# Kernel optimization log

Measured on AMD Instinct MI355X. Metric: run time of the kernel, lower is better.

## Reference

```python
import jax, jax.numpy as jnp
import numpy as np

N = 50000
E = 1_600_000
IN_C = 128
OUT_C = 128


def _glorot(key, shape):
    fan_in, fan_out = shape[0], shape[1]
    s = jnp.sqrt(6.0 / (fan_in + fan_out))
    return jax.random.uniform(key, shape, jnp.float32, -s, s)


def setup_inputs() -> dict:
    key = jax.random.key(0)
    ks = jax.random.split(key, 32)
    inp = {
        'X': jax.random.normal(ks[0], (N, IN_C), jnp.float32),
        'edge_index': jax.random.randint(ks[1], (2, E), 0, N, jnp.int64),
        'edge_weight': jax.random.uniform(ks[2], (E,), jnp.float32),
        'H': jax.random.normal(ks[3], (N, OUT_C), jnp.float32),
        'C': jax.random.normal(ks[4], (N, OUT_C), jnp.float32),
    }
    i = 5
    for g in ('i', 'f', 'c', 'o'):
        inp[f'Wx_{g}'] = _glorot(ks[i], (IN_C, OUT_C)); i += 1
        inp[f'bx_{g}'] = jnp.zeros((OUT_C,), jnp.float32)
        inp[f'Wh_{g}'] = _glorot(ks[i], (OUT_C, OUT_C)); i += 1
        inp[f'bh_{g}'] = jnp.zeros((OUT_C,), jnp.float32)
    for g in ('i', 'f', 'o'):
        inp[f'w_c_{g}'] = _glorot(ks[i], (1, OUT_C)); i += 1
    for g in ('i', 'f', 'c', 'o'):
        inp[f'b_{g}'] = jnp.zeros((1, OUT_C), jnp.float32)
    return inp


def reference(X, edge_index, edge_weight, H, C,
              Wx_i, bx_i, Wh_i, bh_i,
              Wx_f, bx_f, Wh_f, bh_f,
              Wx_c, bx_c, Wh_c, bh_c,
              Wx_o, bx_o, Wh_o, bh_o,
              w_c_i, w_c_f, w_c_o,
              b_i, b_f, b_c, b_o):
    n = X.shape[0]
    src, dst = edge_index[0], edge_index[1]
    # GCN normalization (add_self_loops=False): deg from destination (in-degree)
    deg = jax.ops.segment_sum(edge_weight, dst, num_segments=n)
    dis = jnp.where(deg > 0, jax.lax.rsqrt(jnp.where(deg > 0, deg, 1.0)), 0.0)
    norm = dis[src] * edge_weight * dis[dst]  # [E]

    def gcn(x, W, b):
        xw = x @ W                       # [n, OUT_C]
        msg = xw[src] * norm[:, None]    # gather + scale, [E, OUT_C]
        return jax.ops.segment_sum(msg, dst, num_segments=n) + b

    I = jax.nn.sigmoid(gcn(X, Wx_i, bx_i) + gcn(H, Wh_i, bh_i) + w_c_i * C + b_i)
    Fg = jax.nn.sigmoid(gcn(X, Wx_f, bx_f) + gcn(H, Wh_f, bh_f) + w_c_f * C + b_f)
    T = jnp.tanh(gcn(X, Wx_c, bx_c) + gcn(H, Wh_c, bh_c) + b_c)
    Cn = Fg * C + I * T
    O = jax.nn.sigmoid(gcn(X, Wx_o, bx_o) + gcn(H, Wh_o, bh_o) + w_c_o * Cn + b_o)
    Hn = O * jnp.tanh(Cn)
    return Hn, Cn
```

## Files before the change

### kernel.cpp

```cpp
#include <hip/hip_runtime.h>

__device__ __forceinline__ float bf2f(unsigned short u){
    union { unsigned int i; float f; } v; v.i = ((unsigned int)u) << 16; return v.f;
}
__device__ __forceinline__ unsigned short f2bf(float f){
    union { unsigned int i; float f; } v; v.f = f;
    unsigned int i = v.i;
    unsigned int r = i + 0x7FFFu + ((i >> 16) & 1u);
    return (unsigned short)(r >> 16);
}
__device__ __forceinline__ float sigm(float x){ return 1.0f / (1.0f + __expf(-x)); }

__device__ __forceinline__ float ldsel(const void* p, size_t idx, int fF){
    float r;
    if (fF) r = ((const float*)p)[idx];
    else    r = bf2f(((const unsigned short*)p)[idx]);
    return r;
}

typedef __attribute__((ext_vector_type(8))) short s8v;
typedef __attribute__((ext_vector_type(4))) float f4v;

__global__ void k_detect(const unsigned short* __restrict__ X,
                         const int* __restrict__ ei, int* __restrict__ flags){
    __shared__ int cnt, nz;
    if (threadIdx.x == 0){ cnt = 0; nz = 0; }
    __syncthreads();
    int ok = 0;
    for (int i = threadIdx.x; i < 2048; i += 256){
        int e = (X[i] >> 7) & 0xFF;
        if (e >= 96 && e <= 160) ok++;
    }
    atomicAdd(&cnt, ok);
    int nzl = 0;
    for (int i = threadIdx.x; i < 128; i += 256)
        if (ei[2*i + 1] != 0) nzl++;
    atomicAdd(&nz, nzl);
    __syncthreads();
    if (threadIdx.x == 0){
        flags[0] = (cnt < 1843) ? 1 : 0;
        flags[1] = (nz == 0)   ? 1 : 0;
    }
}

struct PackArgs {
    const void* Wx[4];
    const void* Wh[4];
    const void* bx[4];
    const void* bh[4];
};

__global__ void k_fused1(const void* __restrict__ X, const void* __restrict__ H,
                         uint4* __restrict__ XHb128,
                         const int* __restrict__ ei, const void* __restrict__ ew,
                         unsigned long long* __restrict__ pk,
                         int* __restrict__ off,
                         PackArgs pa, unsigned short* __restrict__ Bp,
                         float* __restrict__ bias,
                         const int* __restrict__ flags,
                         int nbC, int nbT, int E, int N){
    int b = blockIdx.x;
    int fF = flags[0];
    if (b < nbC){
        int base = b*2048 + threadIdx.x;
        int fI = flags[1];
        int dd[8]; unsigned long long pv[8];
#pragma unroll
        for (int k = 0; k < 8; k++){
            int e = base + k*256;
            dd[k] = -1; pv[k] = 0;
            if (e < E){
                dd[k] = fI ? ei[2*(size_t)E + 2*(size_t)e] : ei[(size_t)E + e];
                float w = ldsel(ew, e, fF);
                unsigned int wfix = (unsigned int)(w * 16777216.0f + 0.5f);
                pv[k] = (1ULL << 32) | (unsigned long long)wfix;
            }
        }
#pragma unroll
        for (int k = 0; k < 8; k++){
            int e = base + k*256;
            if (e < E && (unsigned)dd[k] < (unsigned)N){
                unsigned long long old = atomicAdd(&pk[dd[k]], pv[k]);
                off[e] = (int)(old >> 32);
            }
        }
    } else if (b < nbC + nbT){
        int t = (b - nbC)*256 + threadIdx.x;
        if (t >= N*32) return;
        int n = t >> 5, i = t & 31;
        int q = (i < 16) ? i : i - 16;
        uint4 o;
        if (fF){
            const float4* src = (const float4*)((i < 16) ? X : H);
            float4 a = src[(size_t)n*32 + q*2];
            float4 bb = src[(size_t)n*32 + q*2 + 1];
            o.x = ((unsigned int)f2bf(a.y) << 16) | f2bf(a.x);
            o.y = ((unsigned int)f2bf(a.w) << 16) | f2bf(a.z);
            o.z = ((unsigned int)f2bf(bb.y) << 16) | f2bf(bb.x);
            o.w = ((unsigned int)f2bf(bb.w) << 16) | f2bf(bb.z);
        } else {
            const uint4* src = (const uint4*)((i < 16) ? X : H);
            o = src[(size_t)n*16 + q];
        }
        XHb128[(size_t)n*32 + i] = o;
    } else {
        int t = (b - nbC - nbT)*256 + threadIdx.x;
        if (t < 4*8*8*64*8){
            int j    =  t        & 7;
            int lane = (t >> 3)  & 63;
            int kb   = (t >> 9)  & 7;
            int ct   = (t >> 12) & 7;
            int g    = (t >> 15) & 3;
            int k   = kb*32 + (lane >> 4)*8 + j;
            int col = ct*16 + (lane & 15);
            const void* p; size_t idx;
            if (k < 128){ p = pa.Wx[g]; idx = (size_t)k*128 + col; }
            else        { p = pa.Wh[g]; idx = (size_t)(k-128)*128 + col; }
            unsigned short v;
            if (fF) v = f2bf(((const float*)p)[idx]);
            else    v = ((const unsigned short*)p)[idx];
            Bp[t] = v;
        }
        if (t < 512){
            int g = t >> 7, c = t & 127;
            bias[t] = ldsel(pa.bx[g], c, fF) + ldsel(pa.bh[g], c, fF);
        }
    }
}

__global__ void k_scanA(const unsigned long long* __restrict__ pk,
                        int* __restrict__ bsum, int n){
    __shared__ int sh[256];
    int t = threadIdx.x, i = blockIdx.x * 256 + t;
    sh[t] = (i < n) ? (int)(pk[i] >> 32) : 0;
    __syncthreads();
    for (int o = 128; o > 0; o >>= 1){
        if (t < o) sh[t] += sh[t + o];
        __syncthreads();
    }
    if (t == 0) bsum[blockIdx.x] = sh[0];
}
__global__ void k_scanB(const int* __restrict__ bsum, int* __restrict__ bsumoff, int nb){
    __shared__ int sh[256];
    int t = threadIdx.x;
    int v = (t < nb) ? bsum[t] : 0;
    sh[t] = v;
    __syncthreads();
    for (int o = 1; o < 256; o <<= 1){
        int u = (t >= o) ? sh[t - o] : 0;
        __syncthreads();
        sh[t] += u;
        __syncthreads();
    }
    bsumoff[t] = sh[t] - v;
}
__global__ void k_scanC(const unsigned long long* __restrict__ pk,
                        const int* __restrict__ bsumoff,
                        int* __restrict__ rowstart, float* __restrict__ dis, int n){
    __shared__ int sh[256];
    int t = threadIdx.x, i = blockIdx.x * 256 + t;
    unsigned long long pv = (i < n) ? pk[i] : 0ULL;
    int v = (int)(pv >> 32);
    sh[t] = v;
    __syncthreads();
    for (int o = 1; o < 256; o <<= 1){
        int u = (t >= o) ? sh[t - o] : 0;
        __syncthreads();
        sh[t] += u;
        __syncthreads();
    }
    int incl = sh[t];
    if (i < n){
        rowstart[i] = bsumoff[blockIdx.x] + incl - v;
        float dg = (float)(unsigned int)pv * (1.0f/16777216.0f);
        dis[i] = (dg > 0.f) ? rsqrtf(dg) : 0.f;
    }
    if (i == n-1)  rowstart[n] = bsumoff[blockIdx.x] + incl;
}

__global__ void k_scatter(const int* __restrict__ ei, const void* __restrict__ ew,
                          const int* __restrict__ rowstart, const int* __restrict__ off,
                          int2* __restrict__ recs, const int* __restrict__ flags,
                          int E, int N){
    int base = blockIdx.x*1024 + threadIdx.x;
    int fF = flags[0], fI = flags[1];
    int ss[4], dd[4], oo[4]; float wv[4];
#pragma unroll
    for (int k = 0; k < 4; k++){
        int e = base + k*256;
        dd[k] = -1; ss[k] = 0; wv[k] = 0.f; oo[k] = 0;
        if (e < E){
            if (fI){ ss[k] = ei[2*(size_t)e]; dd[k] = ei[2*(size_t)E + 2*(size_t)e]; }
            else   { ss[k] = ei[e];           dd[k] = ei[(size_t)E + e]; }
            oo[k] = off[e];
            if ((unsigned)ss[k] < (unsigned)N) wv[k] = ldsel(ew, e, fF);
            else ss[k] = 0;
        }
    }
#pragma unroll
    for (int k = 0; k < 4; k++){
        if ((unsigned)dd[k] < (unsigned)N){
            int2 r; r.x = ss[k]; r.y = __float_as_int(wv[k]);
            recs[rowstart[dd[k]] + oo[k]] = r;
        }
    }
}

__global__ __launch_bounds__(256)
void k_gather(const int2* __restrict__ recs, const int* __restrict__ rowstart,
              const float* __restrict__ dis, const uint4* __restrict__ XHb128,
              uint4* __restrict__ AXH128, int N){
    int node = (blockIdx.x * 256 + threadIdx.x) >> 6;
    int lane = threadIdx.x & 63;
    if (node >= N) return;
    int half = lane >> 5;
    int sub  = lane & 31;
    int beg = rowstart[node], end = rowstart[node + 1];
    float disd = dis[node];
    float a0=0.f,a1=0.f,a2=0.f,a3=0.f,a4=0.f,a5=0.f,a6=0.f,a7=0.f;

#define ACC8(v, n)                                              \
    a0 += (n) * bf2f((unsigned short)((v).x & 0xffff));         \
    a1 += (n) * bf2f((unsigned short)((v).x >> 16));            \
    a2 += (n) * bf2f((unsigned short)((v).y & 0xffff));         \
    a3 += (n) * bf2f((unsigned short)((v).y >> 16));            \
    a4 += (n) * bf2f((unsigned short)((v).z & 0xffff));         \
    a5 += (n) * bf2f((unsigned short)((v).z >> 16));            \
    a6 += (n) * bf2f((unsigned short)((v).w & 0xffff));         \
    a7 += (n) * bf2f((unsigned short)((v).w >> 16));

    int i = beg;
    for (; i + 7 < end; i += 8){
        int2 rA = recs[i     + half];
        int2 rB = recs[i + 2 + half];
        int2 rC = recs[i + 4 + half];
        int2 rD = recs[i + 6 + half];
        uint4 vA = XHb128[(size_t)rA.x*32 + sub];
        uint4 vB = XHb128[(size_t)rB.x*32 + sub];
        uint4 vC = XHb128[(size_t)rC.x*32 + sub];
        uint4 vD = XHb128[(size_t)rD.x*32 + sub];
        float nA = dis[rA.x] * __int_as_float(rA.y) * disd;
        float nB = dis[rB.x] * __int_as_float(rB.y) * disd;
        float nC = dis[rC.x] * __int_as_float(rC.y) * disd;
        float nD = dis[rD.x] * __int_as_float(rD.y) * disd;
        ACC8(vA, nA);
        ACC8(vB, nB);
        ACC8(vC, nC);
        ACC8(vD, nD);
    }
    for (; i + 1 < end; i += 2){
        int2 rA = recs[i + half];
        uint4 vA = XHb128[(size_t)rA.x*32 + sub];
        float nA = dis[rA.x] * __int_as_float(rA.y) * disd;
        ACC8(vA, nA);
    }
    if (i < end){
        int2 rA = recs[i];
        uint4 vA = XHb128[(size_t)rA.x*32 + sub];
        float nA = (half == 0) ? dis[rA.x] * __int_as_float(rA.y) * disd : 0.f;
        ACC8(vA, nA);
    }
#undef ACC8

    a0 += __shfl_xor(a0, 32, 64);
    a1 += __shfl_xor(a1, 32, 64);
    a2 += __shfl_xor(a2, 32, 64);
    a3 += __shfl_xor(a3, 32, 64);
    a4 += __shfl_xor(a4, 32, 64);
    a5 += __shfl_xor(a5, 32, 64);
    a6 += __shfl_xor(a6, 32, 64);
    a7 += __shfl_xor(a7, 32, 64);

    if (half == 0){
        uint4 o;
        o.x = ((unsigned int)f2bf(a1) << 16) | f2bf(a0);
        o.y = ((unsigned int)f2bf(a3) << 16) | f2bf(a2);
        o.z = ((unsigned int)f2bf(a5) << 16) | f2bf(a4);
        o.w = ((unsigned int)f2bf(a7) << 16) | f2bf(a6);
        AXH128[(size_t)node*32 + sub] = o;
    }
}

struct EpiArgs {
    const void *C, *wci, *wcf, *wco, *bi, *bff, *bc, *bo;
};

__global__ __launch_bounds__(256)
void k_gemm(const unsigned short* __restrict__ AXH,
            const unsigned short* __restrict__ Bp, const float* __restrict__ bias,
            EpiArgs ea, void* __restrict__ outp, const int* __restrict__ flags, int N){
    int tid  = threadIdx.x;
    int w    = tid >> 6, lane = tid & 63;
    int node0 = blockIdx.x * 32;
    int fF = flags[0];

    f4v acc[2][8];
#pragma unroll
    for (int m = 0; m < 2; m++)
#pragma unroll
        for (int c = 0; c < 8; c++) acc[m][c] = (f4v){0.f,0.f,0.f,0.f};

    const unsigned short* a0base = AXH + (size_t)(node0 + (lane & 15))*256 + (lane >> 4)*8;
    const unsigned short* a1base = a0base + 16*256;
#pragma unroll
    for (int kb = 0; kb < 8; kb++){
        s8v af0 = *(const s8v*)(a0base + kb*32);
        s8v af1 = *(const s8v*)(a1base + kb*32);
#pragma unroll
        for (int ct8 = 0; ct8 < 8; ct8++){
            int g = ct8 >> 1, sub = ct8 & 1;
            const s8v bfrag = *(const s8v*)(Bp + g*32768 + (size_t)(w*2 + sub)*4096
                                            + kb*512 + lane*8);
            acc[0][ct8] = __builtin_amdgcn_mfma_f32_16x16x32_bf16(af0, bfrag, acc[0][ct8], 0, 0, 0);
            acc[1][ct8] = __builtin_amdgcn_mfma_f32_16x16x32_bf16(af1, bfrag, acc[1][ct8], 0, 0, 0);
        }
    }

    int q = lane >> 4, cl = lane & 15;
#pragma unroll
    for (int sub = 0; sub < 2; sub++){
        int c = w*32 + sub*16 + cl;
        float bvi = bias[0*128 + c], bvf = bias[1*128 + c];
        float bvc = bias[2*128 + c], bvo = bias[3*128 + c];
        float wci = ldsel(ea.wci, c, fF), wcf = ldsel(ea.wcf, c, fF), wco = ldsel(ea.wco, c, fF);
        float bi  = ldsel(ea.bi, c, fF),  bff = ldsel(ea.bff, c, fF);
        float bc  = ldsel(ea.bc, c, fF),  bo  = ldsel(ea.bo, c, fF);
#pragma unroll
        for (int m = 0; m < 2; m++){
#pragma unroll
            for (int r = 0; r < 4; r++){
                int node = node0 + m*16 + q*4 + r;
                if (node >= N) continue;
                size_t gidx = (size_t)node*128 + c;
                float Cv = ldsel(ea.C, gidx, fF);
                float pi  = acc[m][0+sub][r] + bvi;
                float pf  = acc[m][2+sub][r] + bvf;
                float pcv = acc[m][4+sub][r] + bvc;
                float po  = acc[m][6+sub][r] + bvo;
                float Iv = sigm(pi + wci*Cv + bi);
                float Fv = sigm(pf + wcf*Cv + bff);
                float Tv = tanhf(pcv + bc);
                float Cn = Fv*Cv + Iv*Tv;
                float Ov = sigm(po + wco*Cn + bo);
                float Hn = Ov * tanhf(Cn);
                if (fF){
                    ((float*)outp)[gidx] = Hn;
                    ((float*)outp)[(size_t)N*128 + gidx] = Cn;
                } else {
                    ((unsigned short*)outp)[gidx] = f2bf(Hn);
                    ((unsigned short*)outp)[(size_t)N*128 + gidx] = f2bf(Cn);
                }
            }
        }
    }
}

extern "C" void kernel_launch(void* const* d_in, const int* in_sizes, int n_in,
                              void* d_out, int out_size, void* d_ws, size_t ws_size,
                              hipStream_t stream){
    const void* X  = d_in[0];
    const int*  ei = (const int*)d_in[1];
    const void* ew = d_in[2];
    const void* H  = d_in[3];
    const void* C  = d_in[4];
    const int N = in_sizes[0] / 128;
    const int E = in_sizes[2];

    char* ws = (char*)d_ws;
    unsigned long long* pk = (unsigned long long*)(ws);
    int*   rowstart     = (int*)  (ws + ((size_t)512 << 10));
    int*   bsum         = (int*)  (ws + ((size_t)768 << 10));
    int*   bsumoff      = (int*)  (ws + ((size_t)772 << 10));
    int*   flags        = (int*)  (ws + ((size_t)776 << 10));
    float* dis          = (float*)(ws + ((size_t)780 << 10));
    unsigned short* Bp  = (unsigned short*)(ws + ((size_t)1 << 20));
    float* bias         = (float*)(ws + ((size_t)1 << 20) + ((size_t)256 << 10));
    int*   off          = (int*)  (ws + ((size_t)2 << 20));
    unsigned int* AXH32 = (unsigned int*)(ws + ((size_t)2 << 20));
    int2*  recs         = (int2*) (ws + ((size_t)28 << 20));
    unsigned int* XHb32 = (unsigned int*)(ws + ((size_t)41 << 20));

    hipMemsetAsync(pk, 0, (size_t)512 << 10, stream);
    k_detect<<<1, 256, 0, stream>>>((const unsigned short*)X, ei, flags);

    PackArgs pa;
    pa.Wx[0]=d_in[5];  pa.bx[0]=d_in[6];  pa.Wh[0]=d_in[7];  pa.bh[0]=d_in[8];
    pa.Wx[1]=d_in[9];  pa.bx[1]=d_in[10]; pa.Wh[1]=d_in[11]; pa.bh[1]=d_in[12];
    pa.Wx[2]=d_in[13]; pa.bx[2]=d_in[14]; pa.Wh[2]=d_in[15]; pa.bh[2]=d_in[16];
    pa.Wx[3]=d_in[17]; pa.bx[3]=d_in[18]; pa.Wh[3]=d_in[19]; pa.bh[3]=d_in[20];

    int nbC = (E + 2047)/2048;
    int nbT = (N*32 + 255)/256;
    k_fused1<<<nbC + nbT + 512, 256, 0, stream>>>(X, H, (uint4*)XHb32, ei, ew,
                                                  pk, off, pa, Bp, bias,
                                                  flags, nbC, nbT, E, N);

    int nbA = (N + 255)/256;
    k_scanA<<<nbA, 256, 0, stream>>>(pk, bsum, N);
    k_scanB<<<1, 256, 0, stream>>>(bsum, bsumoff, nbA);
    k_scanC<<<nbA, 256, 0, stream>>>(pk, bsumoff, rowstart, dis, N);

    k_scatter<<<(E + 1023)/1024, 256, 0, stream>>>(ei, ew, rowstart, off, recs, flags, E, N);
    k_gather<<<(N*64 + 255)/256, 256, 0, stream>>>(recs, rowstart, dis,
                                                   (const uint4*)XHb32,
                                                   (uint4*)AXH32, N);

    EpiArgs ea;
    ea.C   = C;
    ea.wci = d_in[21];
    ea.wcf = d_in[22];
    ea.wco = d_in[23];
    ea.bi  = d_in[24];
    ea.bff = d_in[25];
    ea.bc  = d_in[26];
    ea.bo  = d_in[27];
    k_gemm<<<(N + 31)/32, 256, 0, stream>>>((const unsigned short*)AXH32, Bp, bias,
                                            ea, d_out, flags, N);
}
```

Before: 474.9 us.

## Replace CSR scan and scatter with fixed-capacity per-node bins plus overflow list

The degree-count atomic pass now writes each edge record straight into a fixed 64-slot bin per destination node, using the atomic's returned count as the slot. Edges past 64 go to a global overflow list that the gather kernel scans linearly. This removes the three prefix-scan kernels and the separate scatter pass, and with them a second read of the edge list. In exchange the record buffer grows to N*64 entries, bin writes are sparser, and every node's gather walks the whole overflow list. Overflow edges beyond the fixed cap would be silently dropped.

```diff
diff --git a/kernel.cpp b/kernel.cpp
--- a/kernel.cpp
+++ b/kernel.cpp
@@ -20,6 +20,9 @@
 
 typedef __attribute__((ext_vector_type(8))) short s8v;
 typedef __attribute__((ext_vector_type(4))) float f4v;
+
+#define BIN_S   64
+#define OVFCAP  14000
 
 __global__ void k_detect(const unsigned short* __restrict__ X,
                          const int* __restrict__ ei, int* __restrict__ flags){
@@ -54,7 +57,8 @@
                          uint4* __restrict__ XHb128,
                          const int* __restrict__ ei, const void* __restrict__ ew,
                          unsigned long long* __restrict__ pk,
-                         int* __restrict__ off,
+                         int2* __restrict__ recs,
+                         int* __restrict__ novf, int4* __restrict__ ovf,
                          PackArgs pa, unsigned short* __restrict__ Bp,
                          float* __restrict__ bias,
                          const int* __restrict__ flags,
@@ -64,16 +68,19 @@
     if (b < nbC){
         int base = b*2048 + threadIdx.x;
         int fI = flags[1];
-        int dd[8]; unsigned long long pv[8];
+        int dd[8], ss[8]; unsigned long long pv[8]; int wb[8];
 #pragma unroll
         for (int k = 0; k < 8; k++){
             int e = base + k*256;
-            dd[k] = -1; pv[k] = 0;
+            dd[k] = -1; ss[k] = 0; pv[k] = 0; wb[k] = 0;
             if (e < E){
-                dd[k] = fI ? ei[2*(size_t)E + 2*(size_t)e] : ei[(size_t)E + e];
+                if (fI){ ss[k] = ei[2*(size_t)e]; dd[k] = ei[2*(size_t)E + 2*(size_t)e]; }
+                else   { ss[k] = ei[e];           dd[k] = ei[(size_t)E + e]; }
                 float w = ldsel(ew, e, fF);
                 unsigned int wfix = (unsigned int)(w * 16777216.0f + 0.5f);
                 pv[k] = (1ULL << 32) | (unsigned long long)wfix;
+                if ((unsigned)ss[k] < (unsigned)N) wb[k] = __float_as_int(w);
+                else ss[k] = 0;
             }
         }
 #pragma unroll
@@ -81,7 +88,17 @@
             int e = base + k*256;
             if (e < E && (unsigned)dd[k] < (unsigned)N){
                 unsigned long long old = atomicAdd(&pk[dd[k]], pv[k]);
-                off[e] = (int)(old >> 32);
+                int off = (int)(old >> 32);
+                int2 r; r.x = ss[k]; r.y = wb[k];
+                if (off < BIN_S){
+                    recs[(size_t)dd[k]*BIN_S + off] = r;
+                } else {
+                    int slot = atomicAdd(novf, 1);
+                    if (slot < OVFCAP){
+                        int4 o; o.x = dd[k]; o.y = ss[k]; o.z = wb[k]; o.w = 0;
+                        ovf[slot] = o;
+                    }
+                }
             }
         }
     } else if (b < nbC + nbT){
@@ -128,94 +145,28 @@
     }
 }
 
-__global__ void k_scanA(const unsigned long long* __restrict__ pk,
-                        int* __restrict__ bsum, int n){
-    __shared__ int sh[256];
-    int t = threadIdx.x, i = blockIdx.x * 256 + t;
-    sh[t] = (i < n) ? (int)(pk[i] >> 32) : 0;
-    __syncthreads();
-    for (int o = 128; o > 0; o >>= 1){
-        if (t < o) sh[t] += sh[t + o];
-        __syncthreads();
-    }
-    if (t == 0) bsum[blockIdx.x] = sh[0];
-}
-__global__ void k_scanB(const int* __restrict__ bsum, int* __restrict__ bsumoff, int nb){
-    __shared__ int sh[256];
-    int t = threadIdx.x;
-    int v = (t < nb) ? bsum[t] : 0;
-    sh[t] = v;
-    __syncthreads();
-    for (int o = 1; o < 256; o <<= 1){
-        int u = (t >= o) ? sh[t - o] : 0;
-        __syncthreads();
-        sh[t] += u;
-        __syncthreads();
-    }
-    bsumoff[t] = sh[t] - v;
-}
-__global__ void k_scanC(const unsigned long long* __restrict__ pk,
-                        const int* __restrict__ bsumoff,
-                        int* __restrict__ rowstart, float* __restrict__ dis, int n){
-    __shared__ int sh[256];
-    int t = threadIdx.x, i = blockIdx.x * 256 + t;
-    unsigned long long pv = (i < n) ? pk[i] : 0ULL;
-    int v = (int)(pv >> 32);
-    sh[t] = v;
-    __syncthreads();
-    for (int o = 1; o < 256; o <<= 1){
-        int u = (t >= o) ? sh[t - o] : 0;
-        __syncthreads();
-        sh[t] += u;
-        __syncthreads();
-    }
-    int incl = sh[t];
+__global__ void k_dis(const unsigned long long* __restrict__ pk,
+                      float* __restrict__ dis, int n){
+    int i = blockIdx.x*256 + threadIdx.x;
     if (i < n){
-        rowstart[i] = bsumoff[blockIdx.x] + incl - v;
-        float dg = (float)(unsigned int)pv * (1.0f/16777216.0f);
+        float dg = (float)(unsigned int)pk[i] * (1.0f/16777216.0f);
         dis[i] = (dg > 0.f) ? rsqrtf(dg) : 0.f;
     }
-    if (i == n-1)  rowstart[n] = bsumoff[blockIdx.x] + incl;
-}
-
-__global__ void k_scatter(const int* __restrict__ ei, const void* __restrict__ ew,
-                          const int* __restrict__ rowstart, const int* __restrict__ off,
-                          int2* __restrict__ recs, const int* __restrict__ flags,
-                          int E, int N){
-    int base = blockIdx.x*1024 + threadIdx.x;
-    int fF = flags[0], fI = flags[1];
-    int ss[4], dd[4], oo[4]; float wv[4];
-#pragma unroll
-    for (int k = 0; k < 4; k++){
-        int e = base + k*256;
-        dd[k] = -1; ss[k] = 0; wv[k] = 0.f; oo[k] = 0;
-        if (e < E){
-            if (fI){ ss[k] = ei[2*(size_t)e]; dd[k] = ei[2*(size_t)E + 2*(size_t)e]; }
-            else   { ss[k] = ei[e];           dd[k] = ei[(size_t)E + e]; }
-            oo[k] = off[e];
-            if ((unsigned)ss[k] < (unsigned)N) wv[k] = ldsel(ew, e, fF);
-            else ss[k] = 0;
-        }
-    }
-#pragma unroll
-    for (int k = 0; k < 4; k++){
-        if ((unsigned)dd[k] < (unsigned)N){
-            int2 r; r.x = ss[k]; r.y = __float_as_int(wv[k]);
-            recs[rowstart[dd[k]] + oo[k]] = r;
-        }
-    }
 }
 
 __global__ __launch_bounds__(256)
-void k_gather(const int2* __restrict__ recs, const int* __restrict__ rowstart,
+void k_gather(const int2* __restrict__ recs, const unsigned long long* __restrict__ pk,
               const float* __restrict__ dis, const uint4* __restrict__ XHb128,
-              uint4* __restrict__ AXH128, int N){
+              uint4* __restrict__ AXH128, const int* __restrict__ novf,
+              const int4* __restrict__ ovf, int N){
     int node = (blockIdx.x * 256 + threadIdx.x) >> 6;
     int lane = threadIdx.x & 63;
     if (node >= N) return;
     int half = lane >> 5;
     int sub  = lane & 31;
-    int beg = rowstart[node], end = rowstart[node + 1];
+    int cn = (int)(pk[node] >> 32);
+    if (cn > BIN_S) cn = BIN_S;
+    int beg = node*BIN_S, end = beg + cn;
     float disd = dis[node];
     float a0=0.f,a1=0.f,a2=0.f,a3=0.f,a4=0.f,a5=0.f,a6=0.f,a7=0.f;
 
@@ -260,7 +211,6 @@
         float nA = (half == 0) ? dis[rA.x] * __int_as_float(rA.y) * disd : 0.f;
         ACC8(vA, nA);
     }
-#undef ACC8
 
     a0 += __shfl_xor(a0, 32, 64);
     a1 += __shfl_xor(a1, 32, 64);
@@ -272,6 +222,18 @@
     a7 += __shfl_xor(a7, 32, 64);
 
     if (half == 0){
+        int nov = *novf;
+        if (nov > 0){
+            if (nov > OVFCAP) nov = OVFCAP;
+            for (int j = 0; j < nov; j++){
+                int4 r = ovf[j];
+                if (r.x == node){
+                    uint4 v = XHb128[(size_t)r.y*32 + sub];
+                    float n = dis[r.y] * __int_as_float(r.z) * disd;
+                    ACC8(v, n);
+                }
+            }
+        }
         uint4 o;
         o.x = ((unsigned int)f2bf(a1) << 16) | f2bf(a0);
         o.y = ((unsigned int)f2bf(a3) << 16) | f2bf(a2);
@@ -279,6 +241,7 @@
         o.w = ((unsigned int)f2bf(a7) << 16) | f2bf(a6);
         AXH128[(size_t)node*32 + sub] = o;
     }
+#undef ACC8
 }
 
 struct EpiArgs {
@@ -368,16 +331,14 @@
 
     char* ws = (char*)d_ws;
     unsigned long long* pk = (unsigned long long*)(ws);
-    int*   rowstart     = (int*)  (ws + ((size_t)512 << 10));
-    int*   bsum         = (int*)  (ws + ((size_t)768 << 10));
-    int*   bsumoff      = (int*)  (ws + ((size_t)772 << 10));
-    int*   flags        = (int*)  (ws + ((size_t)776 << 10));
-    float* dis          = (float*)(ws + ((size_t)780 << 10));
+    int*   novf         = (int*)  (ws + ((size_t)400 << 10));
+    float* dis          = (float*)(ws + ((size_t)512 << 10));
+    int*   flags        = (int*)  (ws + ((size_t)720 << 10));
+    int4*  ovf          = (int4*) (ws + ((size_t)768 << 10));
     unsigned short* Bp  = (unsigned short*)(ws + ((size_t)1 << 20));
     float* bias         = (float*)(ws + ((size_t)1 << 20) + ((size_t)256 << 10));
-    int*   off          = (int*)  (ws + ((size_t)2 << 20));
     unsigned int* AXH32 = (unsigned int*)(ws + ((size_t)2 << 20));
-    int2*  recs         = (int2*) (ws + ((size_t)28 << 20));
+    int2*  recs         = (int2*) (ws + ((size_t)15 << 20));
     unsigned int* XHb32 = (unsigned int*)(ws + ((size_t)41 << 20));
 
     hipMemsetAsync(pk, 0, (size_t)512 << 10, stream);
@@ -392,18 +353,15 @@
     int nbC = (E + 2047)/2048;
     int nbT = (N*32 + 255)/256;
     k_fused1<<<nbC + nbT + 512, 256, 0, stream>>>(X, H, (uint4*)XHb32, ei, ew,
-                                                  pk, off, pa, Bp, bias,
+                                                  pk, recs, novf, ovf,
+                                                  pa, Bp, bias,
                                                   flags, nbC, nbT, E, N);
 
-    int nbA = (N + 255)/256;
-    k_scanA<<<nbA, 256, 0, stream>>>(pk, bsum, N);
-    k_scanB<<<1, 256, 0, stream>>>(bsum, bsumoff, nbA);
-    k_scanC<<<nbA, 256, 0, stream>>>(pk, bsumoff, rowstart, dis, N);
-
-    k_scatter<<<(E + 1023)/1024, 256, 0, stream>>>(ei, ew, rowstart, off, recs, flags, E, N);
-    k_gather<<<(N*64 + 255)/256, 256, 0, stream>>>(recs, rowstart, dis,
+    k_dis<<<(N + 255)/256, 256, 0, stream>>>(pk, dis, N);
+
+    k_gather<<<(N*64 + 255)/256, 256, 0, stream>>>(recs, pk, dis,
                                                    (const uint4*)XHb32,
-                                                   (uint4*)AXH32, N);
+                                                   (uint4*)AXH32, novf, ovf, N);
 
     EpiArgs ea;
     ea.C   = C;
```

After: 517.2 us. +8.9%, slower.

## Slab feature matrix into 64-byte column chunks and gather per slab pass

Applied to the files above, without the earlier changes.

The bf16 feature table is rewritten into eight column slabs. The gather kernel then processes one slab per pass, with 16 edges in parallel per wave, each edge served by 4 lanes. Keeping each slab small is meant to make the random neighbor reads hit cache instead of DRAM. In exchange, the edge records, degree normalizers and row offsets are reread once per slab. Each neighbor access also becomes a short 64-byte segment, and the inner loop loses its unrolling.

```diff
diff --git a/kernel.cpp b/kernel.cpp
--- a/kernel.cpp
+++ b/kernel.cpp
@@ -50,8 +50,37 @@
     const void* bh[4];
 };
 
+__device__ __forceinline__ void cnt_body(const int* __restrict__ ei,
+                                         const void* __restrict__ ew,
+                                         unsigned long long* __restrict__ pk,
+                                         int* __restrict__ off,
+                                         int fF, int fI,
+                                         int blk, int E, int N){
+    int base = blk*2048 + threadIdx.x;
+    int dd[8]; unsigned long long pv[8];
+#pragma unroll
+    for (int k = 0; k < 8; k++){
+        int e = base + k*256;
+        dd[k] = -1; pv[k] = 0;
+        if (e < E){
+            dd[k] = fI ? ei[2*(size_t)E + 2*(size_t)e] : ei[(size_t)E + e];
+            float w = ldsel(ew, e, fF);
+            unsigned int wfix = (unsigned int)(w * 16777216.0f + 0.5f);
+            pv[k] = (1ULL << 32) | (unsigned long long)wfix;
+        }
+    }
+#pragma unroll
+    for (int k = 0; k < 8; k++){
+        int e = base + k*256;
+        if (e < E && (unsigned)dd[k] < (unsigned)N){
+            unsigned long long old = atomicAdd(&pk[dd[k]], pv[k]);
+            off[e] = (int)(old >> 32);
+        }
+    }
+}
+
 __global__ void k_fused1(const void* __restrict__ X, const void* __restrict__ H,
-                         uint4* __restrict__ XHb128,
+                         uint4* __restrict__ XHs128,
                          const int* __restrict__ ei, const void* __restrict__ ew,
                          unsigned long long* __restrict__ pk,
                          int* __restrict__ off,
@@ -62,28 +91,7 @@
     int b = blockIdx.x;
     int fF = flags[0];
     if (b < nbC){
-        int base = b*2048 + threadIdx.x;
-        int fI = flags[1];
-        int dd[8]; unsigned long long pv[8];
-#pragma unroll
-        for (int k = 0; k < 8; k++){
-            int e = base + k*256;
-            dd[k] = -1; pv[k] = 0;
-            if (e < E){
-                dd[k] = fI ? ei[2*(size_t)E + 2*(size_t)e] : ei[(size_t)E + e];
-                float w = ldsel(ew, e, fF);
-                unsigned int wfix = (unsigned int)(w * 16777216.0f + 0.5f);
-                pv[k] = (1ULL << 32) | (unsigned long long)wfix;
-            }
-        }
-#pragma unroll
-        for (int k = 0; k < 8; k++){
-            int e = base + k*256;
-            if (e < E && (unsigned)dd[k] < (unsigned)N){
-                unsigned long long old = atomicAdd(&pk[dd[k]], pv[k]);
-                off[e] = (int)(old >> 32);
-            }
-        }
+        cnt_body(ei, ew, pk, off, fF, flags[1], b, E, N);
     } else if (b < nbC + nbT){
         int t = (b - nbC)*256 + threadIdx.x;
         if (t >= N*32) return;
@@ -102,7 +110,7 @@
             const uint4* src = (const uint4*)((i < 16) ? X : H);
             o = src[(size_t)n*16 + q];
         }
-        XHb128[(size_t)n*32 + i] = o;
+        XHs128[(size_t)(i >> 2)*N*4 + (size_t)n*4 + (i & 3)] = o;
     } else {
         int t = (b - nbC - nbT)*256 + threadIdx.x;
         if (t < 4*8*8*64*8){
@@ -208,76 +216,55 @@
 
 __global__ __launch_bounds__(256)
 void k_gather(const int2* __restrict__ recs, const int* __restrict__ rowstart,
-              const float* __restrict__ dis, const uint4* __restrict__ XHb128,
+              const float* __restrict__ dis, const uint4* __restrict__ XHs128,
               uint4* __restrict__ AXH128, int N){
-    int node = (blockIdx.x * 256 + threadIdx.x) >> 6;
+    int gw = (blockIdx.x*256 + threadIdx.x) >> 6;
     int lane = threadIdx.x & 63;
-    if (node >= N) return;
-    int half = lane >> 5;
-    int sub  = lane & 31;
+    int pass = gw / N;
+    if (pass >= 8) return;
+    int node = gw - pass*N;
+    int g = lane >> 2;
+    int c = lane & 3;
     int beg = rowstart[node], end = rowstart[node + 1];
     float disd = dis[node];
+    const uint4* slab = XHs128 + (size_t)pass*N*4;
     float a0=0.f,a1=0.f,a2=0.f,a3=0.f,a4=0.f,a5=0.f,a6=0.f,a7=0.f;
 
-#define ACC8(v, n)                                              \
-    a0 += (n) * bf2f((unsigned short)((v).x & 0xffff));         \
-    a1 += (n) * bf2f((unsigned short)((v).x >> 16));            \
-    a2 += (n) * bf2f((unsigned short)((v).y & 0xffff));         \
-    a3 += (n) * bf2f((unsigned short)((v).y >> 16));            \
-    a4 += (n) * bf2f((unsigned short)((v).z & 0xffff));         \
-    a5 += (n) * bf2f((unsigned short)((v).z >> 16));            \
-    a6 += (n) * bf2f((unsigned short)((v).w & 0xffff));         \
-    a7 += (n) * bf2f((unsigned short)((v).w >> 16));
-
-    int i = beg;
-    for (; i + 7 < end; i += 8){
-        int2 rA = recs[i     + half];
-        int2 rB = recs[i + 2 + half];
-        int2 rC = recs[i + 4 + half];
-        int2 rD = recs[i + 6 + half];
-        uint4 vA = XHb128[(size_t)rA.x*32 + sub];
-        uint4 vB = XHb128[(size_t)rB.x*32 + sub];
-        uint4 vC = XHb128[(size_t)rC.x*32 + sub];
-        uint4 vD = XHb128[(size_t)rD.x*32 + sub];
-        float nA = dis[rA.x] * __int_as_float(rA.y) * disd;
-        float nB = dis[rB.x] * __int_as_float(rB.y) * disd;
-        float nC = dis[rC.x] * __int_as_float(rC.y) * disd;
-        float nD = dis[rD.x] * __int_as_float(rD.y) * disd;
-        ACC8(vA, nA);
-        ACC8(vB, nB);
-        ACC8(vC, nC);
-        ACC8(vD, nD);
-    }
-    for (; i + 1 < end; i += 2){
-        int2 rA = recs[i + half];
-        uint4 vA = XHb128[(size_t)rA.x*32 + sub];
-        float nA = dis[rA.x] * __int_as_float(rA.y) * disd;
-        ACC8(vA, nA);
-    }
-    if (i < end){
-        int2 rA = recs[i];
-        uint4 vA = XHb128[(size_t)rA.x*32 + sub];
-        float nA = (half == 0) ? dis[rA.x] * __int_as_float(rA.y) * disd : 0.f;
-        ACC8(vA, nA);
-    }
-#undef ACC8
-
-    a0 += __shfl_xor(a0, 32, 64);
-    a1 += __shfl_xor(a1, 32, 64);
-    a2 += __shfl_xor(a2, 32, 64);
-    a3 += __shfl_xor(a3, 32, 64);
-    a4 += __shfl_xor(a4, 32, 64);
-    a5 += __shfl_xor(a5, 32, 64);
-    a6 += __shfl_xor(a6, 32, 64);
-    a7 += __shfl_xor(a7, 32, 64);
-
-    if (half == 0){
+    for (int i = beg; i < end; i += 16){
+        int idx = i + g;
+        int act = idx < end;
+        int2 r = recs[act ? idx : beg];
+        uint4 v = slab[(size_t)r.x*4 + c];
+        float nv = act ? dis[r.x] * __int_as_float(r.y) * disd : 0.f;
+        a0 += nv * bf2f((unsigned short)(v.x & 0xffff));
+        a1 += nv * bf2f((unsigned short)(v.x >> 16));
+        a2 += nv * bf2f((unsigned short)(v.y & 0xffff));
+        a3 += nv * bf2f((unsigned short)(v.y >> 16));
+        a4 += nv * bf2f((unsigned short)(v.z & 0xffff));
+        a5 += nv * bf2f((unsigned short)(v.z >> 16));
+        a6 += nv * bf2f((unsigned short)(v.w & 0xffff));
+        a7 += nv * bf2f((unsigned short)(v.w >> 16));
+    }
+
+#pragma unroll
+    for (int o = 4; o <= 32; o <<= 1){
+        a0 += __shfl_xor(a0, o, 64);
+        a1 += __shfl_xor(a1, o, 64);
+        a2 += __shfl_xor(a2, o, 64);
+        a3 += __shfl_xor(a3, o, 64);
+        a4 += __shfl_xor(a4, o, 64);
+        a5 += __shfl_xor(a5, o, 64);
+        a6 += __shfl_xor(a6, o, 64);
+        a7 += __shfl_xor(a7, o, 64);
+    }
+
+    if (lane < 4){
         uint4 o;
         o.x = ((unsigned int)f2bf(a1) << 16) | f2bf(a0);
         o.y = ((unsigned int)f2bf(a3) << 16) | f2bf(a2);
         o.z = ((unsigned int)f2bf(a5) << 16) | f2bf(a4);
         o.w = ((unsigned int)f2bf(a7) << 16) | f2bf(a6);
-        AXH128[(size_t)node*32 + sub] = o;
+        AXH128[(size_t)node*32 + pass*4 + lane] = o;
     }
 }
 
@@ -378,7 +365,7 @@
     int*   off          = (int*)  (ws + ((size_t)2 << 20));
     unsigned int* AXH32 = (unsigned int*)(ws + ((size_t)2 << 20));
     int2*  recs         = (int2*) (ws + ((size_t)28 << 20));
-    unsigned int* XHb32 = (unsigned int*)(ws + ((size_t)41 << 20));
+    unsigned int* XHs32 = (unsigned int*)(ws + ((size_t)41 << 20));
 
     hipMemsetAsync(pk, 0, (size_t)512 << 10, stream);
     k_detect<<<1, 256, 0, stream>>>((const unsigned short*)X, ei, flags);
@@ -391,7 +378,7 @@
 
     int nbC = (E + 2047)/2048;
     int nbT = (N*32 + 255)/256;
-    k_fused1<<<nbC + nbT + 512, 256, 0, stream>>>(X, H, (uint4*)XHb32, ei, ew,
+    k_fused1<<<nbC + nbT + 512, 256, 0, stream>>>(X, H, (uint4*)XHs32, ei, ew,
                                                   pk, off, pa, Bp, bias,
                                                   flags, nbC, nbT, E, N);
 
@@ -401,9 +388,10 @@
     k_scanC<<<nbA, 256, 0, stream>>>(pk, bsumoff, rowstart, dis, N);
 
     k_scatter<<<(E + 1023)/1024, 256, 0, stream>>>(ei, ew, rowstart, off, recs, flags, E, N);
-    k_gather<<<(N*64 + 255)/256, 256, 0, stream>>>(recs, rowstart, dis,
-                                                   (const uint4*)XHb32,
-                                                   (uint4*)AXH32, N);
+
+    k_gather<<<2*N, 256, 0, stream>>>(recs, rowstart, dis,
+                                      (const uint4*)XHs32,
+                                      (uint4*)AXH32, N);
 
     EpiArgs ea;
     ea.C   = C;
```

Result: slower. 565.2 us (+19.0%).
